# Optimization experiments

Measured on AMD Instinct MI355X. Metric: run time of the kernel, lower is better.

## Reference

```python
import jax, jax.numpy as jnp
import numpy as np
import math

B, S, D, H, DQ, DV, P = 8, 1024, 512, 8, 64, 64, 32


def _layer_norm(x, g, b, eps=1e-5):
    mu = jnp.mean(x, axis=-1, keepdims=True)
    var = jnp.mean((x - mu) ** 2, axis=-1, keepdims=True)
    return (x - mu) * jax.lax.rsqrt(var + eps) * g + b


def setup_inputs() -> dict:
    key = jax.random.key(0)
    ks = jax.random.split(key, 12)
    s = 0.02
    x = jax.random.normal(ks[0], (B, S, D), dtype=jnp.float32)
    lengths = jax.random.randint(ks[1], (B,), S // 2, S + 1)  # avoid fully-masked rows
    return {
        "x": x,
        "ln_g": jnp.ones((D,), jnp.float32),
        "ln_b": jnp.zeros((D,), jnp.float32),
        "Wk": jax.random.normal(ks[2], (D, H * DQ), jnp.float32) * s,
        "bk": jnp.zeros((H * DQ,), jnp.float32),
        "Wv": jax.random.normal(ks[3], (D, H * DV), jnp.float32) * s,
        "bv": jnp.zeros((H * DV,), jnp.float32),
        "pos": jax.random.normal(ks[4], (1, S, S, P), jnp.float32) * s,  # learned pos table
        "wp": jax.random.normal(ks[5], (P,), jnp.float32) * s,  # map_pos Linear(P,1) weight
        "bp": jnp.zeros((), jnp.float32),  # map_pos bias
        "Wo": jax.random.normal(ks[6], (H * DV, D), jnp.float32) * s,
        "bo": jnp.zeros((D,), jnp.float32),
        "key_value_sequence_lengths": lengths,
    }


def reference(x, ln_g, ln_b, Wk, bk, Wv, bv, pos, wp, bp, Wo, bo, key_value_sequence_lengths):
    # self-attention, encoder (no causal mask), 'kv+pos' branch, eval mode (dropout off)
    xn = _layer_norm(x, ln_g, ln_b)
    k = (xn @ Wk + bk).reshape(B, S, H, DQ).transpose(0, 2, 1, 3)  # [B,H,S,DQ]
    v = (xn @ Wv + bv).reshape(B, S, H, DV).transpose(0, 2, 1, 3)  # [B,H,S,DV]

    # kv+pos: scores use keys twice (tmp = keys since N == M)
    scores = jnp.einsum("bhnd,bhmd->bhnm", k, k) / math.sqrt(H)
    # map_pos(scores[...,None] + pos) == scores * sum(wp) + pos@wp + bp (linear, fused)
    bias = jnp.einsum("qkp,p->qk", pos[0], wp) + bp  # [S,S]
    attn = scores * jnp.sum(wp) + bias[None, None]
    attn = attn / math.sqrt(DQ)

    key_ok = jnp.arange(S)[None, None, None, :] < key_value_sequence_lengths[:, None, None, None]
    attn = jnp.where(key_ok, attn, -jnp.inf)
    probs = jax.nn.softmax(attn, axis=-1)  # [B,H,S,S]

    out = jnp.einsum("bhnm,bhmd->bhnd", probs, v)
    out = out.transpose(0, 2, 1, 3).reshape(B, S, H * DV)
    seq = out @ Wo + bo + x
    return seq, probs
```

## Files before the change

kernel.cpp:

```cpp
#include <hip/hip_runtime.h>
#include <hip/hip_bf16.h>


typedef __attribute__((ext_vector_type(8))) short short8;
typedef __attribute__((ext_vector_type(4))) short short4v;
typedef __attribute__((ext_vector_type(4))) float float4v;

#define MFMA16(a, b, c) __builtin_amdgcn_mfma_f32_16x16x32_bf16((a), (b), (c), 0, 0, 0)

__device__ inline unsigned short f2bf(float f) {
    unsigned u = __builtin_bit_cast(unsigned, f);
    unsigned r = (u + 0x7FFFu + ((u >> 16) & 1u)) >> 16;
    return (unsigned short)r;
}
__device__ inline float bf2f(unsigned short h) {
    unsigned u = ((unsigned)h) << 16;
    return __builtin_bit_cast(float, u);
}

__device__ __forceinline__ void async16(const void* g, void* l) {
    __builtin_amdgcn_global_load_lds(
        (const __attribute__((address_space(1))) unsigned int*)(unsigned long long)g,
        (__attribute__((address_space(3))) unsigned int*)(unsigned)(unsigned long long)l,
        16, 0, 0);
}

__device__ __forceinline__ void barrier_lds() {
    asm volatile("s_waitcnt lgkmcnt(0)" ::: "memory");
    __builtin_amdgcn_sched_barrier(0);
    __builtin_amdgcn_s_barrier();
    __builtin_amdgcn_sched_barrier(0);
}

__global__ __launch_bounds__(256) void ln_kernel(const float* __restrict__ x,
                                                 const float* __restrict__ g,
                                                 const float* __restrict__ b,
                                                 unsigned short* __restrict__ xn) {
    int wave = threadIdx.x >> 6;
    int lane = threadIdx.x & 63;
    size_t row = (size_t)blockIdx.x * 4 + wave;
    const float4* x4 = (const float4*)(x + row * 512);
    float4 v0 = x4[lane];
    float4 v1 = x4[lane + 64];
    float s = v0.x + v0.y + v0.z + v0.w + v1.x + v1.y + v1.z + v1.w;
    for (int o = 32; o; o >>= 1) s += __shfl_xor(s, o);
    float mu = s * (1.0f / 512.0f);
    float d0x = v0.x - mu, d0y = v0.y - mu, d0z = v0.z - mu, d0w = v0.w - mu;
    float d1x = v1.x - mu, d1y = v1.y - mu, d1z = v1.z - mu, d1w = v1.w - mu;
    float q = d0x * d0x + d0y * d0y + d0z * d0z + d0w * d0w +
              d1x * d1x + d1y * d1y + d1z * d1z + d1w * d1w;
    for (int o = 32; o; o >>= 1) q += __shfl_xor(q, o);
    float rs = rsqrtf(q * (1.0f / 512.0f) + 1e-5f);
    const float4* g4 = (const float4*)g;
    const float4* b4 = (const float4*)b;
    float4 g0 = g4[lane], g1 = g4[lane + 64];
    float4 b0 = b4[lane], b1 = b4[lane + 64];
    short4v o0, o1;
    o0[0] = (short)f2bf(d0x * rs * g0.x + b0.x);
    o0[1] = (short)f2bf(d0y * rs * g0.y + b0.y);
    o0[2] = (short)f2bf(d0z * rs * g0.z + b0.z);
    o0[3] = (short)f2bf(d0w * rs * g0.w + b0.w);
    o1[0] = (short)f2bf(d1x * rs * g1.x + b1.x);
    o1[1] = (short)f2bf(d1y * rs * g1.y + b1.y);
    o1[2] = (short)f2bf(d1z * rs * g1.z + b1.z);
    o1[3] = (short)f2bf(d1w * rs * g1.w + b1.w);
    *(short4v*)(xn + row * 512 + lane * 4) = o0;
    *(short4v*)(xn + row * 512 + 256 + lane * 4) = o1;
}

__global__ __launch_bounds__(256) void wconv_kernel(const float* __restrict__ Wk,
                                                    const float* __restrict__ Wv,
                                                    const float* __restrict__ Wo,
                                                    unsigned short* __restrict__ WkT,
                                                    unsigned short* __restrict__ WvT,
                                                    unsigned short* __restrict__ WoT) {
    __shared__ unsigned short t[64 * 66];
    int z = blockIdx.z;
    const float* src = (z == 0) ? Wk : (z == 1) ? Wv : Wo;
    unsigned short* dst = (z == 0) ? WkT : (z == 1) ? WvT : WoT;
    int k0 = blockIdx.x * 64, n0 = blockIdx.y * 64;
    int tx = threadIdx.x & 63, ty = threadIdx.x >> 6;
#pragma unroll
    for (int rr = 0; rr < 16; rr++) {
        int k = ty * 16 + rr;
        float v = src[(size_t)(k0 + k) * 512 + n0 + tx];
        t[tx * 66 + k] = f2bf(v);
    }
    __syncthreads();
#pragma unroll
    for (int rr = 0; rr < 16; rr++) {
        int n = ty * 16 + rr;
        dst[(size_t)(n0 + n) * 512 + k0 + tx] = t[n * 66 + tx];
    }
}

__global__ __launch_bounds__(256) void bias_kernel(const float* __restrict__ pos,
                                                   const float* __restrict__ wp,
                                                   const float* __restrict__ bp,
                                                   unsigned short* __restrict__ biasT) {
    int lane = threadIdx.x & 63;
    int w = threadIdx.x >> 6;
    size_t wbase = ((size_t)blockIdx.x * 4 + w) * 64;
    float4 wv = ((const float4*)wp)[lane & 7];
    float bias0 = bp[0];
#pragma unroll
    for (int t = 0; t < 8; t++) {
        size_t p0 = wbase + (size_t)t * 8;
        const float4* src = (const float4*)(pos + p0 * 32);
        float4 d = src[lane];
        float s = d.x * wv.x + d.y * wv.y + d.z * wv.z + d.w * wv.w;
        s += __shfl_xor(s, 1);
        s += __shfl_xor(s, 2);
        s += __shfl_xor(s, 4);
        if ((lane & 7) == 0) {
            size_t p = p0 + (lane >> 3);
            int q = (int)(p >> 10), k = (int)(p & 1023);
            biasT[(size_t)k * 1024 + q] = f2bf((s + bias0) * 0.125f);
        }
    }
}

__global__ __launch_bounds__(256) void proj_kernel(const unsigned short* __restrict__ xn,
                                                   const unsigned short* __restrict__ WkT,
                                                   const unsigned short* __restrict__ WvT,
                                                   const float* __restrict__ bk,
                                                   const float* __restrict__ bv,
                                                   unsigned short* __restrict__ K,
                                                   unsigned short* __restrict__ Vt) {
    __shared__ unsigned short sa[128 * 32];
    __shared__ unsigned short sb[128 * 32];
    int z = blockIdx.z;
    const unsigned short* Bm = z ? WvT : WkT;
    const float* bias = z ? bv : bk;
    int m0 = blockIdx.y * 128, n0 = blockIdx.x * 128;
    int lane = threadIdx.x & 63, w = threadIdx.x >> 6;
    int l15 = lane & 15, quad = lane >> 4, q8 = quad * 8;
    int wm = w >> 1, wn = w & 1;
    int srow = w * 16 + (lane >> 2);
    int scol = (lane & 3) * 8;
    float4v acc[4][4] = {};
    for (int k0 = 0; k0 < 512; k0 += 32) {
        __syncthreads();
        async16(xn + (size_t)(m0 + srow) * 512 + k0 + scol, &sa[w * 512]);
        async16(xn + (size_t)(m0 + 64 + srow) * 512 + k0 + scol, &sa[2048 + w * 512]);
        async16(Bm + (size_t)(n0 + srow) * 512 + k0 + scol, &sb[w * 512]);
        async16(Bm + (size_t)(n0 + 64 + srow) * 512 + k0 + scol, &sb[2048 + w * 512]);
        __syncthreads();
        short8 af[4], bf[4];
#pragma unroll
        for (int t = 0; t < 4; t++)
            af[t] = *(const short8*)&sa[(wm * 64 + t * 16 + l15) * 32 + q8];
#pragma unroll
        for (int t = 0; t < 4; t++)
            bf[t] = *(const short8*)&sb[(wn * 64 + t * 16 + l15) * 32 + q8];
#pragma unroll
        for (int mt = 0; mt < 4; mt++)
#pragma unroll
            for (int nt = 0; nt < 4; nt++)
                acc[mt][nt] = MFMA16(af[mt], bf[nt], acc[mt][nt]);
    }
#pragma unroll
    for (int mt = 0; mt < 4; mt++)
#pragma unroll
        for (int nt = 0; nt < 4; nt++)
#pragma unroll
            for (int r = 0; r < 4; r++) {
                int m = m0 + wm * 64 + mt * 16 + quad * 4 + r;
                int n = n0 + wn * 64 + nt * 16 + l15;
                float v = acc[mt][nt][r] + bias[n];
                int b = m >> 10, s = m & 1023;
                int h = n >> 6, d = n & 63;
                if (z == 0)
                    K[(((size_t)b * 8 + h) * 1024 + s) * 64 + d] = f2bf(v);
                else
                    Vt[(((size_t)b * 8 + h) * 64 + d) * 1024 + s] = f2bf(v);
            }
}

__global__ __launch_bounds__(256, 4) void attn_kernel(const unsigned short* __restrict__ K,
                                                      const unsigned short* __restrict__ Vt,
                                                      const unsigned short* __restrict__ biasT,
                                                      const float* __restrict__ wp,
                                                      const int* __restrict__ lens,
                                                      float* __restrict__ probs,
                                                      unsigned short* __restrict__ outb) {
    __shared__ unsigned short sc[16 * 1032];
    __shared__ float red[2][4][16];
    int bid = blockIdx.x;
    int bh = bid >> 6, qt = bid & 63;
    int b = bh >> 3, h = bh & 7;
    int q0 = qt * 16;
    int lane = threadIdx.x & 63;
    int w = threadIdx.x >> 6;
    int l15 = lane & 15, quad = lane >> 4;
    int q8 = quad * 8;
    int len = lens[b];

    float swp = 0.f;
#pragma unroll
    for (int j = 0; j < 32; j++) swp += wp[j];
    float c1 = swp * 0.04419417382415922f;

    const unsigned short* Kbh = K + (size_t)bh * 1024 * 64;
    short8 a00 = *(const short8*)(Kbh + (size_t)(q0 + l15) * 64 + q8);
    short8 a01 = *(const short8*)(Kbh + (size_t)(q0 + l15) * 64 + q8 + 32);

    float4v lg[16];
#pragma unroll
    for (int i = 0; i < 16; i++) {
        int n0 = (i * 4 + w) * 16;
        int key = n0 + l15;
        short8 b0 = *(const short8*)(Kbh + (size_t)key * 64 + q8);
        short8 b1 = *(const short8*)(Kbh + (size_t)key * 64 + q8 + 32);
        float4v acc = {};
        acc = MFMA16(a00, b0, acc);
        acc = MFMA16(a01, b1, acc);
        short4v bb4 = *(const short4v*)(biasT + (size_t)key * 1024 + q0 + quad * 4);
        bool ok = key < len;
#pragma unroll
        for (int r = 0; r < 4; r++)
            lg[i][r] = ok ? acc[r] * c1 + bf2f((unsigned short)bb4[r]) : -1e30f;
    }

    float mx[4];
#pragma unroll
    for (int r = 0; r < 4; r++) {
        float m = lg[0][r];
#pragma unroll
        for (int i = 1; i < 16; i++) m = fmaxf(m, lg[i][r]);
        m = fmaxf(m, __shfl_xor(m, 1));
        m = fmaxf(m, __shfl_xor(m, 2));
        m = fmaxf(m, __shfl_xor(m, 4));
        m = fmaxf(m, __shfl_xor(m, 8));
        mx[r] = m;
    }
    if (l15 < 4) {
        float v = (l15 == 0) ? mx[0] : (l15 == 1) ? mx[1] : (l15 == 2) ? mx[2] : mx[3];
        red[0][w][quad * 4 + l15] = v;
    }
    barrier_lds();
#pragma unroll
    for (int r = 0; r < 4; r++) {
        int row = quad * 4 + r;
        mx[r] = fmaxf(fmaxf(red[0][0][row], red[0][1][row]),
                      fmaxf(red[0][2][row], red[0][3][row]));
    }

    float sm[4];
#pragma unroll
    for (int r = 0; r < 4; r++) {
        float s = 0.f;
#pragma unroll
        for (int i = 0; i < 16; i++) {
            float e = __expf(lg[i][r] - mx[r]);
            lg[i][r] = e;
            s += e;
        }
        s += __shfl_xor(s, 1);
        s += __shfl_xor(s, 2);
        s += __shfl_xor(s, 4);
        s += __shfl_xor(s, 8);
        sm[r] = s;
    }
    if (l15 < 4) {
        float v = (l15 == 0) ? sm[0] : (l15 == 1) ? sm[1] : (l15 == 2) ? sm[2] : sm[3];
        red[1][w][quad * 4 + l15] = v;
    }
    barrier_lds();
    float inv[4];
#pragma unroll
    for (int r = 0; r < 4; r++) {
        int row = quad * 4 + r;
        inv[r] = 1.0f / (red[1][0][row] + red[1][1][row] + red[1][2][row] + red[1][3][row]);
    }

#pragma unroll
    for (int i = 0; i < 16; i++) {
        int key = (i * 4 + w) * 16 + l15;
#pragma unroll
        for (int r = 0; r < 4; r++) {
            int row = quad * 4 + r;
            float p = lg[i][r] * inv[r];
            sc[row * 1032 + key] = f2bf(p);
            __builtin_nontemporal_store(p, probs + ((size_t)bh * 1024 + q0 + row) * 1024 + key);
        }
    }
    barrier_lds();

    int nv = w * 16;
    const unsigned short* Vbh = Vt + (size_t)bh * 64 * 1024;
    float4v o0a = {}, o0b = {};
    for (int ks = 0; ks < 32; ks += 2) {
        int k0 = ks * 32;
        short8 bb0 = *(const short8*)(Vbh + (size_t)(nv + l15) * 1024 + k0 + q8);
        short8 p0 = *(const short8*)&sc[l15 * 1032 + k0 + q8];
        short8 bb1 = *(const short8*)(Vbh + (size_t)(nv + l15) * 1024 + k0 + 32 + q8);
        short8 p1 = *(const short8*)&sc[(l15)*1032 + k0 + 32 + q8];
        o0a = MFMA16(p0, bb0, o0a);
        o0b = MFMA16(p1, bb1, o0b);
    }
    float4v o0 = o0a + o0b;
#pragma unroll
    for (int r = 0; r < 4; r++) {
        int row = quad * 4 + r;
        int qa = q0 + row;
        outb[((size_t)b * 1024 + qa) * 512 + h * 64 + nv + l15] = f2bf(o0[r]);
    }
}

__global__ __launch_bounds__(256) void oproj_kernel(const unsigned short* __restrict__ outb,
                                                    const unsigned short* __restrict__ WoT,
                                                    const float* __restrict__ bo,
                                                    const float* __restrict__ x,
                                                    float* __restrict__ seq) {
    __shared__ unsigned short sa[128 * 32];
    __shared__ unsigned short sb[128 * 32];
    int m0 = blockIdx.y * 128, n0 = blockIdx.x * 128;
    int lane = threadIdx.x & 63, w = threadIdx.x >> 6;
    int l15 = lane & 15, quad = lane >> 4, q8 = quad * 8;
    int wm = w >> 1, wn = w & 1;
    int srow = w * 16 + (lane >> 2);
    int scol = (lane & 3) * 8;
    float4v acc[4][4] = {};
    for (int k0 = 0; k0 < 512; k0 += 32) {
        __syncthreads();
        async16(outb + (size_t)(m0 + srow) * 512 + k0 + scol, &sa[w * 512]);
        async16(outb + (size_t)(m0 + 64 + srow) * 512 + k0 + scol, &sa[2048 + w * 512]);
        async16(WoT + (size_t)(n0 + srow) * 512 + k0 + scol, &sb[w * 512]);
        async16(WoT + (size_t)(n0 + 64 + srow) * 512 + k0 + scol, &sb[2048 + w * 512]);
        __syncthreads();
        short8 af[4], bf[4];
#pragma unroll
        for (int t = 0; t < 4; t++)
            af[t] = *(const short8*)&sa[(wm * 64 + t * 16 + l15) * 32 + q8];
#pragma unroll
        for (int t = 0; t < 4; t++)
            bf[t] = *(const short8*)&sb[(wn * 64 + t * 16 + l15) * 32 + q8];
#pragma unroll
        for (int mt = 0; mt < 4; mt++)
#pragma unroll
            for (int nt = 0; nt < 4; nt++)
                acc[mt][nt] = MFMA16(af[mt], bf[nt], acc[mt][nt]);
    }
#pragma unroll
    for (int mt = 0; mt < 4; mt++)
#pragma unroll
        for (int nt = 0; nt < 4; nt++)
#pragma unroll
            for (int r = 0; r < 4; r++) {
                int m = m0 + wm * 64 + mt * 16 + quad * 4 + r;
                int n = n0 + wn * 64 + nt * 16 + l15;
                seq[(size_t)m * 512 + n] = acc[mt][nt][r] + bo[n] + x[(size_t)m * 512 + n];
            }
}

extern "C" void kernel_launch(void* const* d_in, const int* in_sizes, int n_in,
                              void* d_out, int out_size, void* d_ws, size_t ws_size,
                              hipStream_t stream) {
    const float* x    = (const float*)d_in[0];
    const float* ln_g = (const float*)d_in[1];
    const float* ln_b = (const float*)d_in[2];
    const float* Wk   = (const float*)d_in[3];
    const float* bk   = (const float*)d_in[4];
    const float* Wv   = (const float*)d_in[5];
    const float* bv   = (const float*)d_in[6];
    const float* pos  = (const float*)d_in[7];
    const float* wp   = (const float*)d_in[8];
    const float* bp   = (const float*)d_in[9];
    const float* Wo   = (const float*)d_in[10];
    const float* bo   = (const float*)d_in[11];
    const int* lens   = (const int*)d_in[12];

    unsigned short* WkT  = (unsigned short*)d_ws;
    unsigned short* WvT  = WkT + 512 * 512;
    unsigned short* WoT  = WvT + 512 * 512;
    unsigned short* xn   = WoT + 512 * 512;
    unsigned short* Kb   = xn + (size_t)8192 * 512;
    unsigned short* Vt   = Kb + (size_t)64 * 1024 * 64;
    unsigned short* outb = Vt + (size_t)64 * 64 * 1024;
    unsigned short* biasT = outb + (size_t)8192 * 512;

    float* seq = (float*)d_out;
    float* probs = seq + (size_t)8192 * 512;

    hipLaunchKernelGGL(wconv_kernel, dim3(8, 8, 3), dim3(256), 0, stream,
                       Wk, Wv, Wo, WkT, WvT, WoT);
    hipLaunchKernelGGL(ln_kernel, dim3(2048), dim3(256), 0, stream, x, ln_g, ln_b, xn);
    hipLaunchKernelGGL(bias_kernel, dim3(4096), dim3(256), 0, stream, pos, wp, bp, biasT);
    hipLaunchKernelGGL(proj_kernel, dim3(4, 64, 2), dim3(256), 0, stream,
                       xn, WkT, WvT, bk, bv, Kb, Vt);
    hipLaunchKernelGGL(attn_kernel, dim3(4096), dim3(256), 0, stream,
                       Kb, Vt, biasT, wp, lens, probs, outb);
    hipLaunchKernelGGL(oproj_kernel, dim3(4, 64), dim3(256), 0, stream,
                       outb, WoT, bo, x, seq);
}
```

Measured before the change: 561.8 us.

## Transpose QK MFMA output so probs stores are row-contiguous float4

Swaps the MFMA operands so each lane holds one query row and four consecutive keys. Probs can then be written as 16-byte nontemporal vector stores, and the bf16 copy goes to LDS as short4. The row max and row sum reductions become shuffles across quads rather than within a 16-lane group. The block index is remapped so neighbouring blocks share a query tile across heads, and the LDS row padding changes from 1032 to 1028. Bias reads become scalar bf16 loads along the key dimension, so they are more scattered in exchange.

```diff
diff --git a/kernel.cpp b/kernel.cpp
--- a/kernel.cpp
+++ b/kernel.cpp
@@ -184,10 +184,11 @@
                                                       const int* __restrict__ lens,
                                                       float* __restrict__ probs,
                                                       unsigned short* __restrict__ outb) {
-    __shared__ unsigned short sc[16 * 1032];
+    __shared__ unsigned short sc[16 * 1028];
     __shared__ float red[2][4][16];
     int bid = blockIdx.x;
-    int bh = bid >> 6, qt = bid & 63;
+    int bh = ((bid >> 9) << 3) | (bid & 7);
+    int qt = (bid >> 3) & 63;
     int b = bh >> 3, h = bh & 7;
     int q0 = qt * 16;
     int lane = threadIdx.x & 63;
@@ -202,88 +203,67 @@
     float c1 = swp * 0.04419417382415922f;
 
     const unsigned short* Kbh = K + (size_t)bh * 1024 * 64;
-    short8 a00 = *(const short8*)(Kbh + (size_t)(q0 + l15) * 64 + q8);
-    short8 a01 = *(const short8*)(Kbh + (size_t)(q0 + l15) * 64 + q8 + 32);
+    short8 qf0 = *(const short8*)(Kbh + (size_t)(q0 + l15) * 64 + q8);
+    short8 qf1 = *(const short8*)(Kbh + (size_t)(q0 + l15) * 64 + q8 + 32);
 
     float4v lg[16];
 #pragma unroll
     for (int i = 0; i < 16; i++) {
-        int n0 = (i * 4 + w) * 16;
-        int key = n0 + l15;
-        short8 b0 = *(const short8*)(Kbh + (size_t)key * 64 + q8);
-        short8 b1 = *(const short8*)(Kbh + (size_t)key * 64 + q8 + 32);
+        int kb = w * 256 + i * 16;
+        short8 k0f = *(const short8*)(Kbh + (size_t)(kb + l15) * 64 + q8);
+        short8 k1f = *(const short8*)(Kbh + (size_t)(kb + l15) * 64 + q8 + 32);
         float4v acc = {};
-        acc = MFMA16(a00, b0, acc);
-        acc = MFMA16(a01, b1, acc);
-        short4v bb4 = *(const short4v*)(biasT + (size_t)key * 1024 + q0 + quad * 4);
-        bool ok = key < len;
-#pragma unroll
-        for (int r = 0; r < 4; r++)
-            lg[i][r] = ok ? acc[r] * c1 + bf2f((unsigned short)bb4[r]) : -1e30f;
-    }
-
-    float mx[4];
-#pragma unroll
-    for (int r = 0; r < 4; r++) {
-        float m = lg[0][r];
-#pragma unroll
-        for (int i = 1; i < 16; i++) m = fmaxf(m, lg[i][r]);
-        m = fmaxf(m, __shfl_xor(m, 1));
-        m = fmaxf(m, __shfl_xor(m, 2));
-        m = fmaxf(m, __shfl_xor(m, 4));
-        m = fmaxf(m, __shfl_xor(m, 8));
-        mx[r] = m;
-    }
-    if (l15 < 4) {
-        float v = (l15 == 0) ? mx[0] : (l15 == 1) ? mx[1] : (l15 == 2) ? mx[2] : mx[3];
-        red[0][w][quad * 4 + l15] = v;
-    }
+        acc = MFMA16(k0f, qf0, acc);
+        acc = MFMA16(k1f, qf1, acc);
+#pragma unroll
+        for (int r = 0; r < 4; r++) {
+            int key = kb + quad * 4 + r;
+            float bb = bf2f(biasT[(size_t)key * 1024 + q0 + l15]);
+            lg[i][r] = (key < len) ? acc[r] * c1 + bb : -1e30f;
+        }
+    }
+
+    float mx = -1e30f;
+#pragma unroll
+    for (int i = 0; i < 16; i++)
+#pragma unroll
+        for (int r = 0; r < 4; r++) mx = fmaxf(mx, lg[i][r]);
+    mx = fmaxf(mx, __shfl_xor(mx, 16));
+    mx = fmaxf(mx, __shfl_xor(mx, 32));
+    if (lane < 16) red[0][w][lane] = mx;
     barrier_lds();
-#pragma unroll
-    for (int r = 0; r < 4; r++) {
-        int row = quad * 4 + r;
-        mx[r] = fmaxf(fmaxf(red[0][0][row], red[0][1][row]),
-                      fmaxf(red[0][2][row], red[0][3][row]));
-    }
-
-    float sm[4];
-#pragma unroll
-    for (int r = 0; r < 4; r++) {
-        float s = 0.f;
-#pragma unroll
-        for (int i = 0; i < 16; i++) {
-            float e = __expf(lg[i][r] - mx[r]);
+    mx = fmaxf(fmaxf(red[0][0][l15], red[0][1][l15]),
+               fmaxf(red[0][2][l15], red[0][3][l15]));
+
+    float sm = 0.f;
+#pragma unroll
+    for (int i = 0; i < 16; i++)
+#pragma unroll
+        for (int r = 0; r < 4; r++) {
+            float e = __expf(lg[i][r] - mx);
             lg[i][r] = e;
-            s += e;
+            sm += e;
         }
-        s += __shfl_xor(s, 1);
-        s += __shfl_xor(s, 2);
-        s += __shfl_xor(s, 4);
-        s += __shfl_xor(s, 8);
-        sm[r] = s;
-    }
-    if (l15 < 4) {
-        float v = (l15 == 0) ? sm[0] : (l15 == 1) ? sm[1] : (l15 == 2) ? sm[2] : sm[3];
-        red[1][w][quad * 4 + l15] = v;
-    }
+    sm += __shfl_xor(sm, 16);
+    sm += __shfl_xor(sm, 32);
+    if (lane < 16) red[1][w][lane] = sm;
     barrier_lds();
-    float inv[4];
-#pragma unroll
-    for (int r = 0; r < 4; r++) {
-        int row = quad * 4 + r;
-        inv[r] = 1.0f / (red[1][0][row] + red[1][1][row] + red[1][2][row] + red[1][3][row]);
-    }
-
+    float inv = 1.0f / (red[1][0][l15] + red[1][1][l15] + red[1][2][l15] + red[1][3][l15]);
+
+    float* prow = probs + ((size_t)bh * 1024 + q0 + l15) * 1024;
 #pragma unroll
     for (int i = 0; i < 16; i++) {
-        int key = (i * 4 + w) * 16 + l15;
+        int kb = w * 256 + i * 16;
+        float4v pv;
+        short4v pb;
 #pragma unroll
         for (int r = 0; r < 4; r++) {
-            int row = quad * 4 + r;
-            float p = lg[i][r] * inv[r];
-            sc[row * 1032 + key] = f2bf(p);
-            __builtin_nontemporal_store(p, probs + ((size_t)bh * 1024 + q0 + row) * 1024 + key);
+            float p = lg[i][r] * inv;
+            pv[r] = p;
+            pb[r] = (short)f2bf(p);
         }
+        *(short4v*)&sc[l15 * 1028 + kb + quad * 4] = pb;
+        __builtin_nontemporal_store(pv, (float4v*)(prow + kb + quad * 4));
     }
     barrier_lds();
 
@@ -293,9 +273,9 @@
     for (int ks = 0; ks < 32; ks += 2) {
         int k0 = ks * 32;
         short8 bb0 = *(const short8*)(Vbh + (size_t)(nv + l15) * 1024 + k0 + q8);
-        short8 p0 = *(const short8*)&sc[l15 * 1032 + k0 + q8];
+        short8 p0 = *(const short8*)&sc[l15 * 1028 + k0 + q8];
         short8 bb1 = *(const short8*)(Vbh + (size_t)(nv + l15) * 1024 + k0 + 32 + q8);
-        short8 p1 = *(const short8*)&sc[(l15)*1032 + k0 + 32 + q8];
+        short8 p1 = *(const short8*)&sc[l15 * 1028 + k0 + 32 + q8];
         o0a = MFMA16(p0, bb0, o0a);
         o0b = MFMA16(p1, bb1, o0b);
     }
@@ -303,8 +283,7 @@
 #pragma unroll
     for (int r = 0; r < 4; r++) {
         int row = quad * 4 + r;
-        int qa = q0 + row;
-        outb[((size_t)b * 1024 + qa) * 512 + h * 64 + nv + l15] = f2bf(o0[r]);
+        outb[((size_t)b * 1024 + q0 + row) * 512 + h * 64 + nv + l15] = f2bf(o0[r]);
     }
 }
 
```

Result: no change. 559.8 us (-0.4%).
